# Kernel tuning notes

Measured on AMD Instinct MI355X. Metric: run time of the kernel, lower is better.

## Reference

```python
import jax, jax.numpy as jnp
import numpy as np

B, S, D = 4, 2048, 512
H = 8
HD = D // H  # 64


def setup_inputs() -> dict:
    key = jax.random.key(0)
    ks = jax.random.split(key, 11)
    scale = 1.0 / np.sqrt(D)
    inp = {
        "query": jax.random.normal(ks[0], (B, S, D), dtype=jnp.float32),
        "key": jax.random.normal(ks[1], (B, S, D), dtype=jnp.float32),
        "value": jax.random.normal(ks[2], (B, S, D), dtype=jnp.float32),
        "Wq": jax.random.normal(ks[3], (D, D), dtype=jnp.float32) * scale,
        "bq": jnp.zeros((D,), dtype=jnp.float32),
        "Wk": jax.random.normal(ks[4], (D, D), dtype=jnp.float32) * scale,
        "bk": jnp.zeros((D,), dtype=jnp.float32),
        "Wv": jax.random.normal(ks[5], (D, D), dtype=jnp.float32) * scale,
        "bv": jnp.zeros((D,), dtype=jnp.float32),
        "Wo": jax.random.normal(ks[6], (D, D), dtype=jnp.float32) * scale,
        "bo": jnp.zeros((D,), dtype=jnp.float32),
    }
    return inp


def reference(query, key, value, Wq, bq, Wk, bk, Wv, bv, Wo, bo):
    # Linear projections (torch Linear: x @ W.T + b)
    q = (query @ Wq.T + bq).reshape(B, -1, H, HD).transpose(0, 2, 1, 3)  # [B,H,Sq,HD]
    k = (key   @ Wk.T + bk).reshape(B, -1, H, HD).transpose(0, 2, 1, 3)  # [B,H,Sk,HD]
    v = (value @ Wv.T + bv).reshape(B, -1, H, HD).transpose(0, 2, 1, 3)  # [B,H,Sk,HD]

    # Chunked loop in original is mathematically identical to full attention
    scores = jnp.einsum('bhqd,bhkd->bhqk', q, k) / np.sqrt(HD)  # [B,H,Sq,Sk]
    attn = jax.nn.softmax(scores, axis=-1)
    out = jnp.einsum('bhqk,bhkd->bhqd', attn, v)  # [B,H,Sq,HD]
    out = out.transpose(0, 2, 1, 3).reshape(B, -1, D)  # [B,Sq,D]
    return out @ Wo.T + bo
```

## Files before the change

kernel.cpp:

```cpp
#include <hip/hip_runtime.h>
#include <hip/hip_bf16.h>

typedef __attribute__((ext_vector_type(8))) short bf16x8;
typedef __attribute__((ext_vector_type(4))) float f32x4;
typedef __attribute__((ext_vector_type(16))) float f32x16;
typedef __attribute__((ext_vector_type(4))) unsigned int u32x4;

#define MFMA16(a, b, c) __builtin_amdgcn_mfma_f32_16x16x32_bf16((a), (b), (c), 0, 0, 0)
#define MFMA32(a, b, c) __builtin_amdgcn_mfma_f32_32x32x16_bf16((a), (b), (c), 0, 0, 0)

static constexpr int BATCH = 4, S = 2048, DMODEL = 512, H = 8, HD = 64;
static constexpr int M = BATCH * S;

#define WAIT_VM(N) asm volatile("s_waitcnt vmcnt(" #N ")" ::: "memory")
#define SCHEDB() __builtin_amdgcn_sched_barrier(0)

__device__ __forceinline__ float rexp2(float x) {
  float r;
  asm("v_exp_f32 %0, %1" : "=v"(r) : "v"(x));
  return r;
}

__device__ __forceinline__ short f2b(float f) {
  unsigned int u = __builtin_bit_cast(unsigned int, f);
  unsigned int r = (u + 0x7fffu + ((u >> 16) & 1u)) >> 16;
  return (short)r;
}

__device__ __forceinline__ bf16x8 cvt8(const float4& a, const float4& b) {
  bf16x8 r;
  r[0] = f2b(a.x); r[1] = f2b(a.y); r[2] = f2b(a.z); r[3] = f2b(a.w);
  r[4] = f2b(b.x); r[5] = f2b(b.y); r[6] = f2b(b.z); r[7] = f2b(b.w);
  return r;
}

__device__ __forceinline__ void glds16(const void* g, void* l) {
  __builtin_amdgcn_global_load_lds(
      (const __attribute__((address_space(1))) unsigned int*)g,
      (__attribute__((address_space(3))) unsigned int*)l, 16, 0, 0);
}

__global__ __launch_bounds__(256) void convert_all(
    const float* __restrict__ q, const float* __restrict__ k, const float* __restrict__ v,
    const float* __restrict__ Wq, const float* __restrict__ Wk,
    const float* __restrict__ Wv, const float* __restrict__ Wo,
    short* __restrict__ Abq, short* __restrict__ Abk, short* __restrict__ Abv,
    short* __restrict__ Wb) {
  const int bid = blockIdx.x;
  const float* src;
  short* dst;
  int i;
  if (bid < 6144) {
    const int which = bid >> 11;
    const int sub = bid & 2047;
    src = (which == 0) ? q : (which == 1) ? k : v;
    dst = (which == 0) ? Abq : (which == 1) ? Abk : Abv;
    i = (sub * 256 + threadIdx.x) * 8;
  } else {
    const int wb = bid - 6144;
    const int which = wb >> 7;
    const int sub = wb & 127;
    src = (which == 0) ? Wq : (which == 1) ? Wk : (which == 2) ? Wv : Wo;
    dst = Wb + which * (DMODEL * DMODEL);
    i = (sub * 256 + threadIdx.x) * 8;
  }
  float4 a = *(const float4*)&src[i];
  float4 b = *(const float4*)&src[i + 4];
  *(bf16x8*)&dst[i] = cvt8(a, b);
}

__global__ __launch_bounds__(256) void proj_gemm(
    const short* __restrict__ Abq, const short* __restrict__ Abk, const short* __restrict__ Abv,
    const short* __restrict__ Wb,
    const float* __restrict__ bq, const float* __restrict__ bk, const float* __restrict__ bv,
    short* __restrict__ Qp, short* __restrict__ Kp, short* __restrict__ Vp) {
  const int which = blockIdx.y;
  const short* A    = (which == 0) ? Abq : (which == 1) ? Abk : Abv;
  const short* W    = Wb + which * (DMODEL * DMODEL);
  const float* bias = (which == 0) ? bq : (which == 1) ? bk : bv;
  short* dst        = (which == 0) ? Qp : (which == 1) ? Kp : Vp;

  const int tm = blockIdx.x & 63;
  const int tn = blockIdx.x >> 6;
  const int m0 = tm * 128, n0 = tn * 128;
  const int t = threadIdx.x;
  const int lane = t & 63, w = t >> 6;
  const int g = lane >> 4, c = lane & 15;
  const int wr = w >> 1, wc = w & 1;

  __shared__ __align__(16) short SM[3][2 * 128 * 32];

  f32x4 acc[4][4];
  const f32x4 fz = {0.f, 0.f, 0.f, 0.f};
#pragma unroll
  for (int i = 0; i < 4; ++i)
#pragma unroll
    for (int j = 0; j < 4; ++j) acc[i][j] = fz;

  const short* Asrc0 = A + (m0 + w * 16 + (lane >> 2)) * DMODEL + (lane & 3) * 8;
  const short* Asrc1 = Asrc0 + 64 * DMODEL;
  const short* Bsrc0 = W + (n0 + w * 16 + (lane >> 2)) * DMODEL + (lane & 3) * 8;
  const short* Bsrc1 = Bsrc0 + 64 * DMODEL;

#pragma unroll
  for (int tt = 0; tt < 2; ++tt) {
    glds16(Asrc0 + tt * 32, &SM[tt][w * 512]);
    glds16(Asrc1 + tt * 32, &SM[tt][2048 + w * 512]);
    glds16(Bsrc0 + tt * 32, &SM[tt][4096 + w * 512]);
    glds16(Bsrc1 + tt * 32, &SM[tt][4096 + 2048 + w * 512]);
  }

  int ob0 = 0, ob1 = 1, ob2 = 2;
  for (int kt = 0; kt < 16; ++kt) {
    if (kt == 15) { WAIT_VM(0); } else { WAIT_VM(4); }
    __builtin_amdgcn_s_barrier();
    SCHEDB();
    if (kt < 14) {
      const int k0 = (kt + 2) * 32;
      glds16(Asrc0 + k0, &SM[ob2][w * 512]);
      glds16(Asrc1 + k0, &SM[ob2][2048 + w * 512]);
      glds16(Bsrc0 + k0, &SM[ob2][4096 + w * 512]);
      glds16(Bsrc1 + k0, &SM[ob2][4096 + 2048 + w * 512]);
    }
    SCHEDB();

    bf16x8 af[4], bfr[4];
#pragma unroll
    for (int i = 0; i < 4; ++i)
      af[i] = *(const bf16x8*)&SM[ob0][(wr * 64 + i * 16 + c) * 32 + g * 8];
#pragma unroll
    for (int j = 0; j < 4; ++j)
      bfr[j] = *(const bf16x8*)&SM[ob0][4096 + (wc * 64 + j * 16 + c) * 32 + g * 8];
    if (which == 2) {
#pragma unroll
      for (int i = 0; i < 4; ++i)
#pragma unroll
        for (int j = 0; j < 4; ++j)
          acc[i][j] = MFMA16(bfr[j], af[i], acc[i][j]);
    } else {
#pragma unroll
      for (int i = 0; i < 4; ++i)
#pragma unroll
        for (int j = 0; j < 4; ++j)
          acc[i][j] = MFMA16(af[i], bfr[j], acc[i][j]);
    }

    const int tmp = ob0; ob0 = ob1; ob1 = ob2; ob2 = tmp;
  }

  if (which == 2) {
#pragma unroll
    for (int j = 0; j < 4; ++j) {
#pragma unroll
      for (int r = 0; r < 4; ++r) {
        const int n = n0 + wc * 64 + j * 16 + g * 4 + r;
        const int h = n >> 6, hd = n & 63;
        const float bn = bias[n];
#pragma unroll
        for (int i = 0; i < 4; ++i) {
          const int m = m0 + wr * 64 + i * 16 + c;
          const int bb = m >> 11, s = m & (S - 1);
          dst[((bb * H + h) * HD + hd) * S + s] = f2b(acc[i][j][r] + bn);
        }
      }
    }
  } else {
#pragma unroll
    for (int i = 0; i < 4; ++i) {
#pragma unroll
      for (int j = 0; j < 4; ++j) {
        const int n = n0 + wc * 64 + j * 16 + c;
        const int h = n >> 6, hd = n & 63;
        const float bn = bias[n];
#pragma unroll
        for (int r = 0; r < 4; ++r) {
          const int m = m0 + wr * 64 + i * 16 + g * 4 + r;
          const int bb = m >> 11, s = m & (S - 1);
          dst[((bb * H + h) * S + s) * HD + hd] = f2b(acc[i][j][r] + bn);
        }
      }
    }
  }
}

__global__ __launch_bounds__(256) void out_gemm(
    const short* __restrict__ Am, const short* __restrict__ W,
    const float* __restrict__ bias, float* __restrict__ Out) {
  const int tm = blockIdx.x & 63;
  const int tn = blockIdx.x >> 6;
  const int m0 = tm * 128, n0 = tn * 128;
  const int t = threadIdx.x;
  const int lane = t & 63, w = t >> 6;
  const int g = lane >> 4, c = lane & 15;
  const int wr = w >> 1, wc = w & 1;

  __shared__ __align__(16) short SM[4][2 * 128 * 32];

  f32x4 acc[4][4];
  const f32x4 fz = {0.f, 0.f, 0.f, 0.f};
#pragma unroll
  for (int i = 0; i < 4; ++i)
#pragma unroll
    for (int j = 0; j < 4; ++j) acc[i][j] = fz;

  const short* Asrc0 = Am + (m0 + w * 16 + (lane >> 2)) * DMODEL + (lane & 3) * 8;
  const short* Asrc1 = Asrc0 + 64 * DMODEL;
  const short* Bsrc0 = W + (n0 + w * 16 + (lane >> 2)) * DMODEL + (lane & 3) * 8;
  const short* Bsrc1 = Bsrc0 + 64 * DMODEL;

#pragma unroll
  for (int tt = 0; tt < 3; ++tt) {
    glds16(Asrc0 + tt * 32, &SM[tt][w * 512]);
    glds16(Asrc1 + tt * 32, &SM[tt][2048 + w * 512]);
    glds16(Bsrc0 + tt * 32, &SM[tt][4096 + w * 512]);
    glds16(Bsrc1 + tt * 32, &SM[tt][4096 + 2048 + w * 512]);
  }

#pragma unroll 4
  for (int kt = 0; kt < 16; ++kt) {
    if (kt == 15) { WAIT_VM(0); } else if (kt == 14) { WAIT_VM(4); } else { WAIT_VM(8); }
    __builtin_amdgcn_s_barrier();
    SCHEDB();
    if (kt < 13) {
      const int k0 = (kt + 3) * 32;
      glds16(Asrc0 + k0, &SM[(kt + 3) & 3][w * 512]);
      glds16(Asrc1 + k0, &SM[(kt + 3) & 3][2048 + w * 512]);
      glds16(Bsrc0 + k0, &SM[(kt + 3) & 3][4096 + w * 512]);
      glds16(Bsrc1 + k0, &SM[(kt + 3) & 3][4096 + 2048 + w * 512]);
    }
    SCHEDB();

    bf16x8 af[4], bfr[4];
#pragma unroll
    for (int i = 0; i < 4; ++i)
      af[i] = *(const bf16x8*)&SM[kt & 3][(wr * 64 + i * 16 + c) * 32 + g * 8];
#pragma unroll
    for (int j = 0; j < 4; ++j)
      bfr[j] = *(const bf16x8*)&SM[kt & 3][4096 + (wc * 64 + j * 16 + c) * 32 + g * 8];
#pragma unroll
    for (int i = 0; i < 4; ++i)
#pragma unroll
      for (int j = 0; j < 4; ++j)
        acc[i][j] = MFMA16(af[i], bfr[j], acc[i][j]);
  }

#pragma unroll
  for (int i = 0; i < 4; ++i) {
#pragma unroll
    for (int j = 0; j < 4; ++j) {
      const int n = n0 + wc * 64 + j * 16 + c;
      const float bn = bias[n];
#pragma unroll
      for (int r = 0; r < 4; ++r) {
        const int m = m0 + wr * 64 + i * 16 + g * 4 + r;
        Out[m * DMODEL + n] = acc[i][j][r] + bn;
      }
    }
  }
}

__global__ __launch_bounds__(512, 4) void attn_kernel(
    const short* __restrict__ Qp, const short* __restrict__ Kp,
    const short* __restrict__ VTp, short* __restrict__ att) {
  const int bid = blockIdx.x;
  const int swzb = (bid & 7) * 64 + (bid >> 3);
  const int qt = swzb & 15;
  const int bh = swzb >> 4;
  const int b = bh >> 3, h = bh & 7;
  const short* Q  = Qp  + bh * (S * HD);
  const char*  Kg = (const char*)(Kp  + bh * (S * HD));
  const char*  Vg = (const char*)(VTp + bh * (HD * S));

  const int t = threadIdx.x;
  const int lane = t & 63, w = t >> 6;
  const int qi = w >> 1, sj = w & 1;
  const int l31 = lane & 31, hi = lane >> 5;
  const int q0 = qt * 128 + qi * 32;

  __shared__ __align__(16) char smem[2 * 32768];

  const char* ksrc[2];
#pragma unroll
  for (int j = 0; j < 2; ++j) {
    const int rj = w * 8 + j * 4 + (lane >> 4);
    const int tk = (lane & 15) ^ (rj & 15);
    const int kj = 2 * rj + (tk >> 3);
    ksrc[j] = Kg + kj * 128 + (tk & 7) * 16;
  }
  const char* vsrc[2];
#pragma unroll
  for (int j = 0; j < 2; ++j) {
    const int row = w * 8 + j * 4 + (lane >> 4);
    vsrc[j] = Vg + row * 4096 + (((lane & 15) ^ (row & 15)) * 16);
  }

  bf16x8 qf[4];
#pragma unroll
  for (int ks = 0; ks < 4; ++ks)
    qf[ks] = *(const bf16x8*)&Q[(q0 + l31) * HD + ks * 16 + hi * 8];

  f32x16 o0, o1, lsum, fz16;
#pragma unroll
  for (int i = 0; i < 16; ++i) { o0[i] = 0.f; o1[i] = 0.f; lsum[i] = 0.f; fz16[i] = 0.f; }

  const float SCL = 0.18033688011112042f;

  const int kbase = (l31 >> 1) * 256;
  const int k8 = (l31 & 1) << 3;
  const int kx = (l31 >> 1) & 15;
  const int vx = l31 & 15;
  const int sjb = sj * 8192;

  {
    char* nb = smem;
#pragma unroll
    for (int j = 0; j < 2; ++j) glds16(ksrc[j], nb + w * 2048 + j * 1024);
#pragma unroll
    for (int j = 0; j < 2; ++j) glds16(vsrc[j], nb + 16384 + w * 2048 + j * 1024);
  }

  for (int kt = 0; kt < 16; ++kt) {
    WAIT_VM(0);
    __builtin_amdgcn_s_barrier();
    SCHEDB();
    if (kt < 15) {
      char* nb = smem + ((kt + 1) & 1) * 32768;
      const size_t ko = (size_t)(kt + 1) * 16384;
      const size_t vo = (size_t)(kt + 1) * 256;
#pragma unroll
      for (int j = 0; j < 2; ++j) glds16(ksrc[j] + ko, nb + w * 2048 + j * 1024);
#pragma unroll
      for (int j = 0; j < 2; ++j) glds16(vsrc[j] + vo, nb + 16384 + w * 2048 + j * 1024);
    }
    SCHEDB();

    const int cb = (kt & 1) * 32768;

    f32x16 sA, sB;
    __builtin_amdgcn_s_setprio(1);
    {
      const int p0 = ((k8 | hi) ^ kx) * 16;
      sA = MFMA32(*(const bf16x8*)&smem[cb + sjb + kbase + p0],        qf[0], fz16);
      sB = MFMA32(*(const bf16x8*)&smem[cb + sjb + 4096 + kbase + p0], qf[0], fz16);
    }
#pragma unroll
    for (int ks = 1; ks < 4; ++ks) {
      const int p = ((k8 | (ks * 2 + hi)) ^ kx) * 16;
      sA = MFMA32(*(const bf16x8*)&smem[cb + sjb + kbase + p],        qf[ks], sA);
      sB = MFMA32(*(const bf16x8*)&smem[cb + sjb + 4096 + kbase + p], qf[ks], sB);
    }
    __builtin_amdgcn_s_setprio(0);

#pragma unroll
    for (int i = 0; i < 16; ++i) {
      sA[i] = rexp2(sA[i] * SCL);
      sB[i] = rexp2(sB[i] * SCL);
    }

#pragma unroll
    for (int i = 0; i < 16; ++i) lsum[i] += sA[i] + sB[i];

    unsigned int wrdA[8], wrdB[8];
#pragma unroll
    for (int i = 0; i < 8; ++i) {
      asm("v_cvt_pk_bf16_f32 %0, %1, %2" : "=v"(wrdA[i]) : "v"(sA[2 * i]), "v"(sA[2 * i + 1]));
      asm("v_cvt_pk_bf16_f32 %0, %1, %2" : "=v"(wrdB[i]) : "v"(sB[2 * i]), "v"(sB[2 * i + 1]));
    }

    __builtin_amdgcn_s_setprio(1);
#pragma unroll
    for (int ks = 0; ks < 4; ++ks) {
      const int ss = sj * 4 + ks;
      const int i0 = (ks & 1) * 4;
      const unsigned int* lo = (ks < 2) ? wrdA : wrdB;
      unsigned int a0 = lo[i0 + 0], b0 = lo[i0 + 2];
      unsigned int a1 = lo[i0 + 1], b1 = lo[i0 + 3];
      asm("v_permlane32_swap_b32 %0, %1" : "+v"(a0), "+v"(b0));
      asm("v_permlane32_swap_b32 %0, %1" : "+v"(a1), "+v"(b1));
      u32x4 fw;
      fw[0] = a0; fw[1] = a1; fw[2] = b0; fw[3] = b1;
      const bf16x8 pfrag = __builtin_bit_cast(bf16x8, fw);
      const int pv = ((ss * 2 + hi) ^ vx) * 16;
      const bf16x8 va0 = *(const bf16x8*)&smem[cb + 16384 + l31 * 256 + pv];
      const bf16x8 va1 = *(const bf16x8*)&smem[cb + 16384 + (32 + l31) * 256 + pv];
      o0 = MFMA32(va0, pfrag, o0);
      o1 = MFMA32(va1, pfrag, o1);
    }
    __builtin_amdgcn_s_setprio(0);
  }

  float ts[8];
#pragma unroll
  for (int i = 0; i < 8; ++i) ts[i] = lsum[i] + lsum[i + 8];
#pragma unroll
  for (int i = 0; i < 4; ++i) ts[i] = ts[i] + ts[i + 4];
  float lst = (ts[0] + ts[2]) + (ts[1] + ts[3]);
  lst += __shfl_xor(lst, 32, 64);

  __syncthreads();
  float* mrg = (float*)smem;
  if (sj == 1) {
    float* p = mrg + (qi * 64 + lane) * 33;
#pragma unroll
    for (int i = 0; i < 16; ++i) { p[i] = o0[i]; p[16 + i] = o1[i]; }
    p[32] = lst;
  }
  __syncthreads();
  if (sj == 0) {
    const float* p = mrg + (qi * 64 + lane) * 33;
    const float inv = 1.0f / (lst + p[32]);
    short* arow = att + (b * S + q0 + l31) * DMODEL + h * HD;
#pragma unroll
    for (int dt = 0; dt < 2; ++dt) {
#pragma unroll
      for (int rr = 0; rr < 4; ++rr) {
        const int i0 = 4 * rr;
        const float* po = p + dt * 16;
        float v0 = ((dt ? o1[i0 + 0] : o0[i0 + 0]) + po[i0 + 0]) * inv;
        float v1 = ((dt ? o1[i0 + 1] : o0[i0 + 1]) + po[i0 + 1]) * inv;
        float v2 = ((dt ? o1[i0 + 2] : o0[i0 + 2]) + po[i0 + 2]) * inv;
        float v3 = ((dt ? o1[i0 + 3] : o0[i0 + 3]) + po[i0 + 3]) * inv;
        unsigned int w0, w1;
        asm("v_cvt_pk_bf16_f32 %0, %1, %2" : "=v"(w0) : "v"(v0), "v"(v1));
        asm("v_cvt_pk_bf16_f32 %0, %1, %2" : "=v"(w1) : "v"(v2), "v"(v3));
        uint2 pk2;
        pk2.x = w0; pk2.y = w1;
        *(uint2*)&arow[dt * 32 + rr * 8 + hi * 4] = pk2;
      }
    }
  }
}

extern "C" void kernel_launch(void* const* d_in, const int* in_sizes, int n_in,
                              void* d_out, int out_size, void* d_ws, size_t ws_size,
                              hipStream_t stream) {
  const float* query = (const float*)d_in[0];
  const float* key_  = (const float*)d_in[1];
  const float* value = (const float*)d_in[2];
  const float* Wq = (const float*)d_in[3];
  const float* bq = (const float*)d_in[4];
  const float* Wk = (const float*)d_in[5];
  const float* bk = (const float*)d_in[6];
  const float* Wv = (const float*)d_in[7];
  const float* bv = (const float*)d_in[8];
  const float* Wo = (const float*)d_in[9];
  const float* bo = (const float*)d_in[10];
  float* out = (float*)d_out;

  char* ws = (char*)d_ws;
  const size_t WB_BYTES  = (size_t)4 * DMODEL * DMODEL * 2;
  const size_t MAT_BYTES = (size_t)M * DMODEL * 2;
  short* Wb  = (short*)ws;
  short* Qp  = (short*)(ws + WB_BYTES);
  short* Kp  = (short*)(ws + WB_BYTES + MAT_BYTES);
  short* Vp  = (short*)(ws + WB_BYTES + 2 * MAT_BYTES);
  short* att = (short*)(ws + WB_BYTES + 3 * MAT_BYTES);
  short* Abq = (short*)(ws + WB_BYTES + 4 * MAT_BYTES);
  short* Abk = (short*)(ws + WB_BYTES + 5 * MAT_BYTES);
  short* Abv = att;

  convert_all<<<dim3(6656), 256, 0, stream>>>(query, key_, value, Wq, Wk, Wv, Wo,
                                              Abq, Abk, Abv, Wb);
  proj_gemm<<<dim3(256, 3), 256, 0, stream>>>(Abq, Abk, Abv, Wb, bq, bk, bv, Qp, Kp, Vp);
  attn_kernel<<<dim3(512), 512, 0, stream>>>(Qp, Kp, Vp, att);
  out_gemm<<<dim3(256), 256, 0, stream>>>(att, Wb + 3 * DMODEL * DMODEL, bo, out);
}
```

Measured before the change: 93.66 us.

## Fuse fp32-to-bf16 activation conversion into projection GEMM tile loads

Drops the separate pass that converted query/key/value to bf16 in global memory. The projection GEMM now loads fp32 activation tiles straight into LDS with an XOR-swizzled layout and converts them to bf16 while building MFMA fragments. Only the weights still go through a small conversion kernel. This removes one full read/write round trip of the activations and a launch, but doubles the A-tile LDS footprint and adds conversion ALU work inside the GEMM loop.

```diff
diff --git a/kernel.cpp b/kernel.cpp
--- a/kernel.cpp
+++ b/kernel.cpp
@@ -40,42 +40,26 @@
       (__attribute__((address_space(3))) unsigned int*)l, 16, 0, 0);
 }
 
-__global__ __launch_bounds__(256) void convert_all(
-    const float* __restrict__ q, const float* __restrict__ k, const float* __restrict__ v,
+__global__ __launch_bounds__(256) void convert_w(
     const float* __restrict__ Wq, const float* __restrict__ Wk,
     const float* __restrict__ Wv, const float* __restrict__ Wo,
-    short* __restrict__ Abq, short* __restrict__ Abk, short* __restrict__ Abv,
     short* __restrict__ Wb) {
-  const int bid = blockIdx.x;
-  const float* src;
-  short* dst;
-  int i;
-  if (bid < 6144) {
-    const int which = bid >> 11;
-    const int sub = bid & 2047;
-    src = (which == 0) ? q : (which == 1) ? k : v;
-    dst = (which == 0) ? Abq : (which == 1) ? Abk : Abv;
-    i = (sub * 256 + threadIdx.x) * 8;
-  } else {
-    const int wb = bid - 6144;
-    const int which = wb >> 7;
-    const int sub = wb & 127;
-    src = (which == 0) ? Wq : (which == 1) ? Wk : (which == 2) ? Wv : Wo;
-    dst = Wb + which * (DMODEL * DMODEL);
-    i = (sub * 256 + threadIdx.x) * 8;
-  }
+  const float* src = (blockIdx.y == 0) ? Wq : (blockIdx.y == 1) ? Wk
+                   : (blockIdx.y == 2) ? Wv : Wo;
+  short* dst = Wb + blockIdx.y * (DMODEL * DMODEL);
+  int i = (blockIdx.x * 256 + threadIdx.x) * 8;
   float4 a = *(const float4*)&src[i];
   float4 b = *(const float4*)&src[i + 4];
   *(bf16x8*)&dst[i] = cvt8(a, b);
 }
 
 __global__ __launch_bounds__(256) void proj_gemm(
-    const short* __restrict__ Abq, const short* __restrict__ Abk, const short* __restrict__ Abv,
+    const float* __restrict__ Aq, const float* __restrict__ Ak, const float* __restrict__ Av,
     const short* __restrict__ Wb,
     const float* __restrict__ bq, const float* __restrict__ bk, const float* __restrict__ bv,
     short* __restrict__ Qp, short* __restrict__ Kp, short* __restrict__ Vp) {
   const int which = blockIdx.y;
-  const short* A    = (which == 0) ? Abq : (which == 1) ? Abk : Abv;
+  const float* A    = (which == 0) ? Aq : (which == 1) ? Ak : Av;
   const short* W    = Wb + which * (DMODEL * DMODEL);
   const float* bias = (which == 0) ? bq : (which == 1) ? bk : bv;
   short* dst        = (which == 0) ? Qp : (which == 1) ? Kp : Vp;
@@ -88,7 +72,7 @@
   const int g = lane >> 4, c = lane & 15;
   const int wr = w >> 1, wc = w & 1;
 
-  __shared__ __align__(16) short SM[3][2 * 128 * 32];
+  __shared__ __align__(16) char SM[3][24576];
 
   f32x4 acc[4][4];
   const f32x4 fz = {0.f, 0.f, 0.f, 0.f};
@@ -97,40 +81,52 @@
 #pragma unroll
     for (int j = 0; j < 4; ++j) acc[i][j] = fz;
 
-  const short* Asrc0 = A + (m0 + w * 16 + (lane >> 2)) * DMODEL + (lane & 3) * 8;
-  const short* Asrc1 = Asrc0 + 64 * DMODEL;
+  const float* Asrc[4];
+#pragma unroll
+  for (int j = 0; j < 4; ++j)
+    Asrc[j] = A + (m0 + w * 32 + j * 8 + (lane >> 3)) * DMODEL +
+              (((lane & 7) ^ (lane >> 3)) * 4);
   const short* Bsrc0 = W + (n0 + w * 16 + (lane >> 2)) * DMODEL + (lane & 3) * 8;
   const short* Bsrc1 = Bsrc0 + 64 * DMODEL;
 
 #pragma unroll
   for (int tt = 0; tt < 2; ++tt) {
-    glds16(Asrc0 + tt * 32, &SM[tt][w * 512]);
-    glds16(Asrc1 + tt * 32, &SM[tt][2048 + w * 512]);
-    glds16(Bsrc0 + tt * 32, &SM[tt][4096 + w * 512]);
-    glds16(Bsrc1 + tt * 32, &SM[tt][4096 + 2048 + w * 512]);
+#pragma unroll
+    for (int j = 0; j < 4; ++j)
+      glds16(Asrc[j] + tt * 32, &SM[tt][w * 4096 + j * 1024]);
+    glds16(Bsrc0 + tt * 32, &SM[tt][16384 + w * 1024]);
+    glds16(Bsrc1 + tt * 32, &SM[tt][16384 + 4096 + w * 1024]);
   }
 
   int ob0 = 0, ob1 = 1, ob2 = 2;
   for (int kt = 0; kt < 16; ++kt) {
-    if (kt == 15) { WAIT_VM(0); } else { WAIT_VM(4); }
+    if (kt == 15) { WAIT_VM(0); } else { WAIT_VM(6); }
     __builtin_amdgcn_s_barrier();
     SCHEDB();
     if (kt < 14) {
       const int k0 = (kt + 2) * 32;
-      glds16(Asrc0 + k0, &SM[ob2][w * 512]);
-      glds16(Asrc1 + k0, &SM[ob2][2048 + w * 512]);
-      glds16(Bsrc0 + k0, &SM[ob2][4096 + w * 512]);
-      glds16(Bsrc1 + k0, &SM[ob2][4096 + 2048 + w * 512]);
+#pragma unroll
+      for (int j = 0; j < 4; ++j)
+        glds16(Asrc[j] + k0, &SM[ob2][w * 4096 + j * 1024]);
+      glds16(Bsrc0 + k0, &SM[ob2][16384 + w * 1024]);
+      glds16(Bsrc1 + k0, &SM[ob2][16384 + 4096 + w * 1024]);
     }
     SCHEDB();
 
     bf16x8 af[4], bfr[4];
 #pragma unroll
-    for (int i = 0; i < 4; ++i)
-      af[i] = *(const bf16x8*)&SM[ob0][(wr * 64 + i * 16 + c) * 32 + g * 8];
-#pragma unroll
-    for (int j = 0; j < 4; ++j)
-      bfr[j] = *(const bf16x8*)&SM[ob0][4096 + (wc * 64 + j * 16 + c) * 32 + g * 8];
+    for (int i = 0; i < 4; ++i) {
+      const int row = wr * 64 + i * 16 + c;
+      const int key = row & 7;
+      const float4 f0 = *(const float4*)&SM[ob0][row * 128 + ((g * 2) ^ key) * 16];
+      const float4 f1 = *(const float4*)&SM[ob0][row * 128 + ((g * 2 + 1) ^ key) * 16];
+      af[i] = cvt8(f0, f1);
+    }
+#pragma unroll
+    for (int j = 0; j < 4; ++j) {
+      const int row = wc * 64 + j * 16 + c;
+      bfr[j] = *(const bf16x8*)&SM[ob0][16384 + row * 64 + g * 16];
+    }
     if (which == 2) {
 #pragma unroll
       for (int i = 0; i < 4; ++i)
@@ -455,13 +451,9 @@
   short* Kp  = (short*)(ws + WB_BYTES + MAT_BYTES);
   short* Vp  = (short*)(ws + WB_BYTES + 2 * MAT_BYTES);
   short* att = (short*)(ws + WB_BYTES + 3 * MAT_BYTES);
-  short* Abq = (short*)(ws + WB_BYTES + 4 * MAT_BYTES);
-  short* Abk = (short*)(ws + WB_BYTES + 5 * MAT_BYTES);
-  short* Abv = att;
-
-  convert_all<<<dim3(6656), 256, 0, stream>>>(query, key_, value, Wq, Wk, Wv, Wo,
-                                              Abq, Abk, Abv, Wb);
-  proj_gemm<<<dim3(256, 3), 256, 0, stream>>>(Abq, Abk, Abv, Wb, bq, bk, bv, Qp, Kp, Vp);
+
+  convert_w<<<dim3(128, 4), 256, 0, stream>>>(Wq, Wk, Wv, Wo, Wb);
+  proj_gemm<<<dim3(256, 3), 256, 0, stream>>>(query, key_, value, Wb, bq, bk, bv, Qp, Kp, Vp);
   attn_kernel<<<dim3(512), 512, 0, stream>>>(Qp, Kp, Vp, att);
   out_gemm<<<dim3(256), 256, 0, stream>>>(att, Wb + 3 * DMODEL * DMODEL, bo, out);
 }
```

Result: slower. 104.5 us (+11.5%).
